# Kernel tuning notes

Hardware: AMD Instinct MI355X
Metric: run time of the kernel (lower is better)

The kernel has to match this reference:

```python
import jax, jax.numpy as jnp
import numpy as np

# Static configuration (matches init_kwargs / input_specs)
F, K = 64, 3            # filters, kernel_size
B, H, W, C = 64, 32, 32, 8
S = 1                   # strides (VALID padding, stride 1)
O1, O2 = H - K + 1, W - K + 1
L = O1 * O2             # output_lenght
N = H * W               # Right_shape[0]*Right_shape[1] (VALID -> no pad)
NTRI = K * ((K - 1) // 2) * K // K * 1  # per-filter strict-triangular count
NTRI = K * (K - 1) // 2  # = k*floor((k-1)/2) for odd k (3 for k=3)


def _phi_n_indices():
    """Column indices of the sparse phi operator, per set_indices_phi.
    For VALID/stride-1 the window start for output i=(r,c) is r*W + c.
    Returns int array (L, K*K) with n = block*W + start + j."""
    r = np.arange(O1)
    c = np.arange(O2)
    start = (r[:, None] * W + c[None, :]).reshape(L)          # (L,)
    blk = np.arange(K)[:, None] * W + np.arange(K)[None, :]   # (K,K)
    n = start[:, None, None] + blk[None]                      # (L,K,K)
    return n.reshape(L, K * K)

_N_IDX = jnp.asarray(_phi_n_indices())          # (L, K*K) static
_TI, _TJ = np.triu_indices(K, 1)                # strict upper, row-major
_LI, _LJ = np.tril_indices(K, -1)               # strict lower, row-major


def setup_inputs() -> dict:
    key = jax.random.key(0)
    ks = jax.random.split(key, 6)
    u = lambda k_, shp: jax.random.uniform(k_, shp, jnp.float32, -0.05, 0.05)
    return {
        "inputs": jax.random.normal(ks[0], (B, H, W, C), jnp.float32),
        "omega_diag": u(ks[1], (F, K)),
        "omega_triu": u(ks[2], (1, F * NTRI)),
        "omega_tril": u(ks[3], (1, F * NTRI)),
        "lambda_in": u(ks[4], (K, 1)),
        "lambda_out": u(ks[5], (1, K)),
        "use_encode": jnp.ones((1, N), jnp.float32),
        "use_decode": jnp.zeros((L, 1), jnp.float32),
    }


def reference(inputs, omega_diag, omega_triu, omega_tril,
              lambda_in, lambda_out, use_encode, use_decode):
    # flatten + matrix_pad (identity for VALID) + channel mean
    up = inputs.reshape(B, N, C).mean(axis=-1)                # (B, N)

    # Assemble omega = tril + diag + triu, per filter (F,K,K)
    omega = jnp.zeros((F, K, K), inputs.dtype)
    omega = omega.at[:, _TI, _TJ].set(omega_triu.reshape(F, NTRI))
    omega = omega.at[:, _LI, _LJ].set(omega_tril.reshape(F, NTRI))
    omega = omega.at[:, jnp.arange(K), jnp.arange(K)].set(omega_diag)
    base = omega * (lambda_in - lambda_out)                   # (F,K,K)

    # Scatter base into the dense phi operator (F, L, N)
    vals = jnp.broadcast_to(base.reshape(F, 1, K * K), (F, L, K * K))
    kernel = jnp.zeros((F, L, N), inputs.dtype)
    kernel = kernel.at[:, jnp.arange(L)[:, None], _N_IDX].set(vals)

    # kernel @ diag(encode) - diag(decode) @ kernel  (column/row scaling)
    kernel = kernel * use_encode[0][None, None, :] \
             - use_decode[:, 0][None, :, None] * kernel

    # (F,L,N) x (B,N) -> (B,L,F), then to image layout
    out = jnp.einsum('fln,bn->blf', kernel, up)
    out = out.reshape(B, O1, O2, F)
    return jax.nn.relu(out)
```

## Files before the change

kernel.cpp:

```cpp
#include <hip/hip_runtime.h>


#define SPL 30

__global__ __launch_bounds__(256) void spectral_conv_kernel(
    const float* __restrict__ inputs,
    const float* __restrict__ om_diag,
    const float* __restrict__ om_triu,
    const float* __restrict__ om_tril,
    const float* __restrict__ lam_in,
    const float* __restrict__ lam_out,
    const float* __restrict__ enc,
    const float* __restrict__ dec,
    float* __restrict__ out)
{
    __shared__ float4 up4[257];
    __shared__ float4 ue4[257];
    float* up_s = (float*)up4;
    float* ue_s = (float*)ue4;

    const int tid   = threadIdx.x;
    const int b     = (int)blockIdx.x & 63;
    const int split = (int)blockIdx.x >> 6;

    const float* img = inputs + (size_t)b * 8192;
    #pragma unroll
    for (int k = 0; k < 4; ++k) {
        int m = tid + 256 * k;
        const float4* p4 = (const float4*)(img + m * 8);
        float4 a = p4[0];
        float4 q = p4[1];
        float u = (a.x + a.y + a.z + a.w + q.x + q.y + q.z + q.w) * 0.125f;
        up_s[m] = u;
        ue_s[m] = u * enc[m];
    }
    __syncthreads();

    const int f   = tid & 63;
    const int wid = tid >> 6;
    const float li0 = lam_in[0],  li1 = lam_in[1],  li2 = lam_in[2];
    const float lo0 = lam_out[0], lo1 = lam_out[1], lo2 = lam_out[2];
    const float w00 = om_diag[f * 3 + 0] * (li0 - lo0);
    const float w01 = om_triu[f * 3 + 0] * (li0 - lo1);
    const float w02 = om_triu[f * 3 + 1] * (li0 - lo2);
    const float w10 = om_tril[f * 3 + 0] * (li1 - lo0);
    const float w11 = om_diag[f * 3 + 1] * (li1 - lo1);
    const float w12 = om_triu[f * 3 + 2] * (li1 - lo2);
    const float w20 = om_tril[f * 3 + 1] * (li2 - lo0);
    const float w21 = om_tril[f * 3 + 2] * (li2 - lo1);
    const float w22 = om_diag[f * 3 + 2] * (li2 - lo2);

    const int sg = split * 4 + wid;
    const int r0 = (sg >> 3) * 2;
    const int cb = (sg & 7) * 4;

    float Ur[4][8], Er[4][8];
    #pragma unroll
    for (int rw = 0; rw < 4; ++rw) {
        int b4 = (((r0 + rw) << 5) + cb) >> 2;
        *(float4*)&Ur[rw][0] = up4[b4];
        *(float4*)&Ur[rw][4] = up4[b4 + 1];
        *(float4*)&Er[rw][0] = ue4[b4];
        *(float4*)&Er[rw][4] = ue4[b4 + 1];
    }

    const int p0 = r0 * 30 + cb;
    float* outb = out + (size_t)b * (900 * 64);

    #pragma unroll
    for (int q = 0; q < 4; ++q) {
        if (cb + q < 30) {
            float s1 = w00 * Er[0][q];
            float s2 = w00 * Ur[0][q];
            s1 = fmaf(w01, Er[0][q+1], s1);  s2 = fmaf(w01, Ur[0][q+1], s2);
            s1 = fmaf(w02, Er[0][q+2], s1);  s2 = fmaf(w02, Ur[0][q+2], s2);
            s1 = fmaf(w10, Er[1][q  ], s1);  s2 = fmaf(w10, Ur[1][q  ], s2);
            s1 = fmaf(w11, Er[1][q+1], s1);  s2 = fmaf(w11, Ur[1][q+1], s2);
            s1 = fmaf(w12, Er[1][q+2], s1);  s2 = fmaf(w12, Ur[1][q+2], s2);
            s1 = fmaf(w20, Er[2][q  ], s1);  s2 = fmaf(w20, Ur[2][q  ], s2);
            s1 = fmaf(w21, Er[2][q+1], s1);  s2 = fmaf(w21, Ur[2][q+1], s2);
            s1 = fmaf(w22, Er[2][q+2], s1);  s2 = fmaf(w22, Ur[2][q+2], s2);
            float dl0 = dec[p0 + q];
            outb[(p0 + q) * 64 + f] = fmaxf(fmaf(-dl0, s2, s1), 0.0f);

            float t1 = w00 * Er[1][q];
            float t2 = w00 * Ur[1][q];
            t1 = fmaf(w01, Er[1][q+1], t1);  t2 = fmaf(w01, Ur[1][q+1], t2);
            t1 = fmaf(w02, Er[1][q+2], t1);  t2 = fmaf(w02, Ur[1][q+2], t2);
            t1 = fmaf(w10, Er[2][q  ], t1);  t2 = fmaf(w10, Ur[2][q  ], t2);
            t1 = fmaf(w11, Er[2][q+1], t1);  t2 = fmaf(w11, Ur[2][q+1], t2);
            t1 = fmaf(w12, Er[2][q+2], t1);  t2 = fmaf(w12, Ur[2][q+2], t2);
            t1 = fmaf(w20, Er[3][q  ], t1);  t2 = fmaf(w20, Ur[3][q  ], t2);
            t1 = fmaf(w21, Er[3][q+1], t1);  t2 = fmaf(w21, Ur[3][q+1], t2);
            t1 = fmaf(w22, Er[3][q+2], t1);  t2 = fmaf(w22, Ur[3][q+2], t2);
            float dl1 = dec[p0 + 30 + q];
            outb[(p0 + 30 + q) * 64 + f] = fmaxf(fmaf(-dl1, t2, t1), 0.0f);
        }
    }
}

extern "C" void kernel_launch(void* const* d_in, const int* in_sizes, int n_in,
                              void* d_out, int out_size, void* d_ws, size_t ws_size,
                              hipStream_t stream) {
    const float* inputs  = (const float*)d_in[0];
    const float* om_diag = (const float*)d_in[1];
    const float* om_triu = (const float*)d_in[2];
    const float* om_tril = (const float*)d_in[3];
    const float* lam_in  = (const float*)d_in[4];
    const float* lam_out = (const float*)d_in[5];
    const float* enc     = (const float*)d_in[6];
    const float* dec     = (const float*)d_in[7];
    float* out = (float*)d_out;

    dim3 grid(64 * SPL);
    dim3 block(256);
    spectral_conv_kernel<<<grid, block, 0, stream>>>(
        inputs, om_diag, om_triu, om_tril, lam_in, lam_out, enc, dec, out);
}
```

Baseline: 76.80 us.

## Load only the input rows each stripe needs instead of the whole image

Each block now handles a two-output-row stripe and loads and channel-averages only the four input rows it needs. Previously every block reduced the full image. Loads use one float4 per thread with a lane shuffle, and the padding in shared memory is zeroed. The grid is halved so each wave computes eight columns, and a launch-bounds occupancy hint is added. This removes heavy redundant global reads and reduction work at the cost of fewer, longer blocks.

```diff
diff --git a/kernel.cpp b/kernel.cpp
--- a/kernel.cpp
+++ b/kernel.cpp
@@ -1,9 +1,9 @@
 #include <hip/hip_runtime.h>
 
 
-#define SPL 30
+#define STRIPES 15
 
-__global__ __launch_bounds__(256) void spectral_conv_kernel(
+__global__ __launch_bounds__(256, 4) void spectral_conv_kernel(
     const float* __restrict__ inputs,
     const float* __restrict__ om_diag,
     const float* __restrict__ om_triu,
@@ -14,27 +14,20 @@
     const float* __restrict__ dec,
     float* __restrict__ out)
 {
-    __shared__ float4 up4[257];
-    __shared__ float4 ue4[257];
+    __shared__ float4 up4[34];
+    __shared__ float4 ue4[34];
     float* up_s = (float*)up4;
     float* ue_s = (float*)ue4;
 
-    const int tid   = threadIdx.x;
-    const int b     = (int)blockIdx.x & 63;
-    const int split = (int)blockIdx.x >> 6;
+    const int tid    = threadIdx.x;
+    const int b      = (int)blockIdx.x & 63;
+    const int stripe = (int)blockIdx.x >> 6;
+    const int r0     = stripe * 2;
 
-    const float* img = inputs + (size_t)b * 8192;
-    #pragma unroll
-    for (int k = 0; k < 4; ++k) {
-        int m = tid + 256 * k;
-        const float4* p4 = (const float4*)(img + m * 8);
-        float4 a = p4[0];
-        float4 q = p4[1];
-        float u = (a.x + a.y + a.z + a.w + q.x + q.y + q.z + q.w) * 0.125f;
-        up_s[m] = u;
-        ue_s[m] = u * enc[m];
-    }
-    __syncthreads();
+    const float4* src = (const float4*)(inputs + ((size_t)b * 1024 + (size_t)r0 * 32) * 8);
+    float4 v = src[tid];
+    float s = v.x + v.y + v.z + v.w;
+    s += __shfl_xor(s, 1);
 
     const int f   = tid & 63;
     const int wid = tid >> 6;
@@ -50,51 +43,64 @@
     const float w21 = om_tril[f * 3 + 2] * (li2 - lo1);
     const float w22 = om_diag[f * 3 + 2] * (li2 - lo2);
 
-    const int sg = split * 4 + wid;
-    const int r0 = (sg >> 3) * 2;
-    const int cb = (sg & 7) * 4;
+    if ((tid & 1) == 0) {
+        int m = tid >> 1;
+        float u = s * 0.125f;
+        up_s[m] = u;
+        ue_s[m] = u * enc[r0 * 32 + m];
+    }
+    if (tid < 8) { up_s[128 + tid] = 0.0f; ue_s[128 + tid] = 0.0f; }
+    __syncthreads();
 
-    float Ur[4][8], Er[4][8];
-    #pragma unroll
-    for (int rw = 0; rw < 4; ++rw) {
-        int b4 = (((r0 + rw) << 5) + cb) >> 2;
-        *(float4*)&Ur[rw][0] = up4[b4];
-        *(float4*)&Ur[rw][4] = up4[b4 + 1];
-        *(float4*)&Er[rw][0] = ue4[b4];
-        *(float4*)&Er[rw][4] = ue4[b4 + 1];
-    }
-
-    const int p0 = r0 * 30 + cb;
+    const int cb    = wid * 8;
+    const int prow0 = r0 * 30;
     float* outb = out + (size_t)b * (900 * 64);
 
     #pragma unroll
-    for (int q = 0; q < 4; ++q) {
-        if (cb + q < 30) {
-            float s1 = w00 * Er[0][q];
-            float s2 = w00 * Ur[0][q];
-            s1 = fmaf(w01, Er[0][q+1], s1);  s2 = fmaf(w01, Ur[0][q+1], s2);
-            s1 = fmaf(w02, Er[0][q+2], s1);  s2 = fmaf(w02, Ur[0][q+2], s2);
-            s1 = fmaf(w10, Er[1][q  ], s1);  s2 = fmaf(w10, Ur[1][q  ], s2);
-            s1 = fmaf(w11, Er[1][q+1], s1);  s2 = fmaf(w11, Ur[1][q+1], s2);
-            s1 = fmaf(w12, Er[1][q+2], s1);  s2 = fmaf(w12, Ur[1][q+2], s2);
-            s1 = fmaf(w20, Er[2][q  ], s1);  s2 = fmaf(w20, Ur[2][q  ], s2);
-            s1 = fmaf(w21, Er[2][q+1], s1);  s2 = fmaf(w21, Ur[2][q+1], s2);
-            s1 = fmaf(w22, Er[2][q+2], s1);  s2 = fmaf(w22, Ur[2][q+2], s2);
-            float dl0 = dec[p0 + q];
-            outb[(p0 + q) * 64 + f] = fmaxf(fmaf(-dl0, s2, s1), 0.0f);
+    for (int g = 0; g < 2; ++g) {
+        const int c0 = cb + g * 4;
 
-            float t1 = w00 * Er[1][q];
-            float t2 = w00 * Ur[1][q];
-            t1 = fmaf(w01, Er[1][q+1], t1);  t2 = fmaf(w01, Ur[1][q+1], t2);
-            t1 = fmaf(w02, Er[1][q+2], t1);  t2 = fmaf(w02, Ur[1][q+2], t2);
-            t1 = fmaf(w10, Er[2][q  ], t1);  t2 = fmaf(w10, Ur[2][q  ], t2);
-            t1 = fmaf(w11, Er[2][q+1], t1);  t2 = fmaf(w11, Ur[2][q+1], t2);
-            t1 = fmaf(w12, Er[2][q+2], t1);  t2 = fmaf(w12, Ur[2][q+2], t2);
-            t1 = fmaf(w20, Er[3][q  ], t1);  t2 = fmaf(w20, Ur[3][q  ], t2);
-            t1 = fmaf(w21, Er[3][q+1], t1);  t2 = fmaf(w21, Ur[3][q+1], t2);
-            t1 = fmaf(w22, Er[3][q+2], t1);  t2 = fmaf(w22, Ur[3][q+2], t2);
-            float dl1 = dec[p0 + 30 + q];
-            outb[(p0 + 30 + q) * 64 + f] = fmaxf(fmaf(-dl1, t2, t1), 0.0f);
+        float Ur[4][8], Er[4][8];
+        #pragma unroll
+        for (int rw = 0; rw < 4; ++rw) {
+            int b4 = (rw * 32 + c0) >> 2;
+            *(float4*)&Ur[rw][0] = up4[b4];
+            *(float4*)&Ur[rw][4] = up4[b4 + 1];
+            *(float4*)&Er[rw][0] = ue4[b4];
+            *(float4*)&Er[rw][4] = ue4[b4 + 1];
+        }
+
+        #pragma unroll
+        for (int q = 0; q < 4; ++q) {
+            const int col = c0 + q;
+            if (col < 30) {
+                float s1 = w00 * Er[0][q];
+                float s2 = w00 * Ur[0][q];
+                s1 = fmaf(w01, Er[0][q+1], s1);  s2 = fmaf(w01, Ur[0][q+1], s2);
+                s1 = fmaf(w02, Er[0][q+2], s1);  s2 = fmaf(w02, Ur[0][q+2], s2);
+                s1 = fmaf(w10, Er[1][q  ], s1);  s2 = fmaf(w10, Ur[1][q  ], s2);
+                s1 = fmaf(w11, Er[1][q+1], s1);  s2 = fmaf(w11, Ur[1][q+1], s2);
+                s1 = fmaf(w12, Er[1][q+2], s1);  s2 = fmaf(w12, Ur[1][q+2], s2);
+                s1 = fmaf(w20, Er[2][q  ], s1);  s2 = fmaf(w20, Ur[2][q  ], s2);
+                s1 = fmaf(w21, Er[2][q+1], s1);  s2 = fmaf(w21, Ur[2][q+1], s2);
+                s1 = fmaf(w22, Er[2][q+2], s1);  s2 = fmaf(w22, Ur[2][q+2], s2);
+                const int p0 = prow0 + col;
+                float dl0 = dec[p0];
+                outb[(size_t)p0 * 64 + f] = fmaxf(fmaf(-dl0, s2, s1), 0.0f);
+
+                float t1 = w00 * Er[1][q];
+                float t2 = w00 * Ur[1][q];
+                t1 = fmaf(w01, Er[1][q+1], t1);  t2 = fmaf(w01, Ur[1][q+1], t2);
+                t1 = fmaf(w02, Er[1][q+2], t1);  t2 = fmaf(w02, Ur[1][q+2], t2);
+                t1 = fmaf(w10, Er[2][q  ], t1);  t2 = fmaf(w10, Ur[2][q  ], t2);
+                t1 = fmaf(w11, Er[2][q+1], t1);  t2 = fmaf(w11, Ur[2][q+1], t2);
+                t1 = fmaf(w12, Er[2][q+2], t1);  t2 = fmaf(w12, Ur[2][q+2], t2);
+                t1 = fmaf(w20, Er[3][q  ], t1);  t2 = fmaf(w20, Ur[3][q  ], t2);
+                t1 = fmaf(w21, Er[3][q+1], t1);  t2 = fmaf(w21, Ur[3][q+1], t2);
+                t1 = fmaf(w22, Er[3][q+2], t1);  t2 = fmaf(w22, Ur[3][q+2], t2);
+                float dl1 = dec[p0 + 30];
+                outb[(size_t)(p0 + 30) * 64 + f] = fmaxf(fmaf(-dl1, t2, t1), 0.0f);
+            }
         }
     }
 }
@@ -112,7 +118,7 @@
     const float* dec     = (const float*)d_in[7];
     float* out = (float*)d_out;
 
-    dim3 grid(64 * SPL);
+    dim3 grid(64 * STRIPES);
     dim3 block(256);
     spectral_conv_kernel<<<grid, block, 0, stream>>>(
         inputs, om_diag, om_triu, om_tril, lam_in, lam_out, enc, dec, out);
```

After: 76.15 us. No clear change (-0.9%).
